# Kernel optimization log

Hardware: AMD Instinct MI355X
Metric: run time of the kernel (lower is better)

Reference implementation:

```python
import jax, jax.numpy as jnp
import numpy as np

NUM_FEATURES = 128
NUM_RADIAL = 6
NUM_ATOM_TYPES = 95
N_ATOMS = 100000
N_EDGES = 1000000


def setup_inputs() -> dict:
    key = jax.random.key(0)
    ks = jax.random.split(key, 8)
    Z = jax.random.randint(ks[0], (N_ATOMS,), 0, NUM_ATOM_TYPES, dtype=jnp.int32)
    rbf = jax.random.normal(ks[1], (N_EDGES, NUM_RADIAL), dtype=jnp.float32)
    idnb_i = jax.random.randint(ks[2], (N_EDGES,), 0, N_ATOMS, dtype=jnp.int32)
    idnb_j = jax.random.randint(ks[3], (N_EDGES,), 0, N_ATOMS, dtype=jnp.int32)
    # parameters
    s3 = np.sqrt(3.0).astype(np.float32)
    embeddings = jax.random.uniform(ks[4], (NUM_ATOM_TYPES, NUM_FEATURES), jnp.float32, -s3, s3)
    W_rbf = jax.random.normal(ks[5], (NUM_RADIAL, NUM_FEATURES), dtype=jnp.float32) * 0.3
    b_rbf = jnp.zeros((NUM_FEATURES,), jnp.float32)
    W = jax.random.normal(ks[6], (2 * NUM_FEATURES + NUM_RADIAL * 0 + 2 * NUM_FEATURES // (2 * NUM_FEATURES) * 0 + 2 * NUM_FEATURES + NUM_FEATURES - 2 * NUM_FEATURES, NUM_FEATURES), dtype=jnp.float32)  # placeholder, replaced below
    W = jax.random.normal(ks[6], (2 * NUM_FEATURES + NUM_FEATURES, NUM_FEATURES), dtype=jnp.float32) * 0.05  # (3F, F)
    b = jnp.zeros((NUM_FEATURES,), jnp.float32)
    return {"Z": Z, "rbf": rbf, "idnb_i": idnb_i, "idnb_j": idnb_j,
            "embeddings": embeddings, "W_rbf": W_rbf, "b_rbf": b_rbf, "W": W, "b": b}


def reference(Z, rbf, idnb_i, idnb_j, embeddings, W_rbf, b_rbf, W, b):
    act = jax.nn.swish
    # dense_rbf: [E, num_radial] -> [E, F]
    rbf_h = act(rbf @ W_rbf + b_rbf)
    # gather atom embeddings by atomic number, then by edge endpoints
    x = embeddings[Z]            # [N_atoms, F]
    x1 = x[idnb_i]               # [E, F]
    x2 = x[idnb_j]               # [E, F]
    h = jnp.concatenate([x1, x2, rbf_h], axis=-1)  # [E, 3F]
    return act(h @ W + b)        # [E, F]
```

## Files before the change

kernel.cpp:

```cpp
#include <hip/hip_runtime.h>
#include <hip/hip_bf16.h>
#include <stdint.h>

#define F 128
#define R 6
#define NTYPES 95
#define MTILE 128
#define HPAD 136

typedef short bf16x8 __attribute__((ext_vector_type(8)));
typedef float floatx4 __attribute__((ext_vector_type(4)));

__device__ __forceinline__ unsigned short f2bf(float x) {
    union { float f; unsigned u; } cv; cv.f = x;
    unsigned u = cv.u;
    return (unsigned short)((u + 0x7FFFu + ((u >> 16) & 1u)) >> 16);
}

__device__ __forceinline__ float swishf(float x) {
    return x / (1.0f + __expf(-x));
}

__global__ void prep_kernel(const float* __restrict__ emb,
                            const float* __restrict__ W,
                            float* __restrict__ embW,
                            unsigned short* __restrict__ w2t) {
    int t = threadIdx.x;
    int b = blockIdx.x;
    if (b < NTYPES) {
        int c = t >> 7, f = t & 127;
        const float* er = emb + b * F;
        const float* Wc = W + c * F * F;
        float a = 0.f;
        #pragma unroll 8
        for (int k = 0; k < F; ++k) a = __builtin_fmaf(er[k], Wc[k * F + f], a);
        embW[b * 256 + c * F + f] = a;
    } else {
        int idx = (b - NTYPES) * 256 + t;
        int n = idx >> 7, k = idx & 127;
        w2t[n * F + k] = f2bf(W[(256 + k) * F + n]);
    }
}

__global__ __launch_bounds__(256) void
edge_kernel(const int* __restrict__ Z,
            const float* __restrict__ rbf,
            const int* __restrict__ idnb_i,
            const int* __restrict__ idnb_j,
            const float* __restrict__ W_rbf,
            const float* __restrict__ b_rbf,
            const float* __restrict__ bvec,
            const float* __restrict__ embW,
            const unsigned short* __restrict__ w2t,
            float* __restrict__ out,
            int E) {
    __shared__ __align__(16) short h_bf[MTILE * HPAD];
    __shared__ float rbf_s[MTILE * R];
    __shared__ int zi_s[MTILE];
    __shared__ int zj_s[MTILE];
    __shared__ float bs[F];

    int t = threadIdx.x;
    int blk = blockIdx.x;
    long ebase = (long)blk * MTILE;

    #pragma unroll
    for (int i = 0; i < 3; ++i) {
        int idx = i * 256 + t;
        long g = ebase * R + idx;
        rbf_s[idx] = (g < (long)E * R) ? rbf[g] : 0.f;
    }
    if (t < MTILE) {
        long e = ebase + t;
        long ec = (e < (long)E) ? e : 0;
        zi_s[t] = Z[idnb_i[ec]];
        zj_s[t] = Z[idnb_j[ec]];
    }
    if (t < F) bs[t] = bvec[t];

    int fpair = t & 63;
    int f0 = fpair * 2;
    float wr0[R], wr1[R];
    #pragma unroll
    for (int r = 0; r < R; ++r) {
        wr0[r] = W_rbf[r * F + f0];
        wr1[r] = W_rbf[r * F + f0 + 1];
    }
    float brb0 = b_rbf[f0], brb1 = b_rbf[f0 + 1];

    __syncthreads();

    int eg = t >> 6;
    for (int it = 0; it < 32; ++it) {
        int e = eg * 32 + it;
        const float* rp = rbf_s + e * R;
        float v0 = brb0, v1 = brb1;
        #pragma unroll
        for (int r = 0; r < R; ++r) {
            float rv = rp[r];
            v0 = __builtin_fmaf(rv, wr0[r], v0);
            v1 = __builtin_fmaf(rv, wr1[r], v1);
        }
        v0 = swishf(v0); v1 = swishf(v1);
        unsigned packed = (unsigned)f2bf(v0) | ((unsigned)f2bf(v1) << 16);
        *(unsigned*)(&h_bf[e * HPAD + f0]) = packed;
    }

    __syncthreads();

    int w = t >> 6;
    int lid = t & 63;
    int quad = lid >> 4;
    int l15 = lid & 15;
    int wbase = w * 32;

    floatx4 acc[2][8];
    #pragma unroll
    for (int rt = 0; rt < 2; ++rt)
        #pragma unroll
        for (int c = 0; c < 8; ++c)
            acc[rt][c] = (floatx4){0.f, 0.f, 0.f, 0.f};

    const bf16x8* w2v = (const bf16x8*)w2t;
    #pragma unroll
    for (int ks = 0; ks < 4; ++ks) {
        bf16x8 a0 = *(const bf16x8*)(&h_bf[(wbase + l15) * HPAD + ks * 32 + quad * 8]);
        bf16x8 a1 = *(const bf16x8*)(&h_bf[(wbase + 16 + l15) * HPAD + ks * 32 + quad * 8]);
        #pragma unroll
        for (int c = 0; c < 8; ++c) {
            bf16x8 bfr = w2v[(c * 16 + l15) * 16 + ks * 4 + quad];
            acc[0][c] = __builtin_amdgcn_mfma_f32_16x16x32_bf16(a0, bfr, acc[0][c], 0, 0, 0);
            acc[1][c] = __builtin_amdgcn_mfma_f32_16x16x32_bf16(a1, bfr, acc[1][c], 0, 0, 0);
        }
    }

    #pragma unroll
    for (int rt = 0; rt < 2; ++rt) {
        #pragma unroll
        for (int rg = 0; rg < 4; ++rg) {
            int e_loc = wbase + rt * 16 + quad * 4 + rg;
            long e_g = ebase + e_loc;
            bool ok = e_g < (long)E;
            int zi = zi_s[e_loc], zj = zj_s[e_loc];
            const float* p0 = embW + zi * 256;
            const float* p1 = embW + zj * 256 + F;
            float* op = out + e_g * F;
            #pragma unroll
            for (int c = 0; c < 8; ++c) {
                int f = c * 16 + l15;
                float v = acc[rt][c][rg] + p0[f] + p1[f] + bs[f];
                v = swishf(v);
                if (ok) op[f] = v;
            }
        }
    }
}

extern "C" void kernel_launch(void* const* d_in, const int* in_sizes, int n_in,
                              void* d_out, int out_size, void* d_ws, size_t ws_size,
                              hipStream_t stream) {
    const int*   Z     = (const int*)d_in[0];
    const float* rbf   = (const float*)d_in[1];
    const int*   id_i  = (const int*)d_in[2];
    const int*   id_j  = (const int*)d_in[3];
    const float* emb   = (const float*)d_in[4];
    const float* W_rbf = (const float*)d_in[5];
    const float* b_rbf = (const float*)d_in[6];
    const float* W     = (const float*)d_in[7];
    const float* bvec  = (const float*)d_in[8];
    float* out = (float*)d_out;
    int E = in_sizes[2];

    float* embW = (float*)d_ws;
    unsigned short* w2t = (unsigned short*)((char*)d_ws + 97280);

    prep_kernel<<<NTYPES + 64, 256, 0, stream>>>(emb, W, embW, w2t);
    int grid = (E + MTILE - 1) / MTILE;
    edge_kernel<<<grid, 256, 0, stream>>>(Z, rbf, id_i, id_j, W_rbf, b_rbf, bvec,
                                          embW, w2t, out, E);
}
```

Baseline: 710.3 us.

## Stage MFMA outputs through LDS for coalesced float4 epilogue stores and fold bias

```diff
diff --git a/kernel.cpp b/kernel.cpp
--- a/kernel.cpp
+++ b/kernel.cpp
@@ -7,6 +7,7 @@
 #define NTYPES 95
 #define MTILE 128
 #define HPAD 136
+#define SPAD 132
 
 typedef short bf16x8 __attribute__((ext_vector_type(8)));
 typedef float floatx4 __attribute__((ext_vector_type(4)));
@@ -18,11 +19,12 @@
 }
 
 __device__ __forceinline__ float swishf(float x) {
-    return x / (1.0f + __expf(-x));
+    return x * __builtin_amdgcn_rcpf(1.0f + __expf(-x));
 }
 
 __global__ void prep_kernel(const float* __restrict__ emb,
                             const float* __restrict__ W,
+                            const float* __restrict__ bvec,
                             float* __restrict__ embW,
                             unsigned short* __restrict__ w2t) {
     int t = threadIdx.x;
@@ -34,6 +36,7 @@
         float a = 0.f;
         #pragma unroll 8
         for (int k = 0; k < F; ++k) a = __builtin_fmaf(er[k], Wc[k * F + f], a);
+        if (c == 0) a += bvec[f];
         embW[b * 256 + c * F + f] = a;
     } else {
         int idx = (b - NTYPES) * 256 + t;
@@ -49,20 +52,20 @@
             const int* __restrict__ idnb_j,
             const float* __restrict__ W_rbf,
             const float* __restrict__ b_rbf,
-            const float* __restrict__ bvec,
             const float* __restrict__ embW,
             const unsigned short* __restrict__ w2t,
             float* __restrict__ out,
             int E) {
-    __shared__ __align__(16) short h_bf[MTILE * HPAD];
+    __shared__ __align__(16) union {
+        short h[MTILE * HPAD];
+        float s[64 * SPAD];
+    } shm;
     __shared__ float rbf_s[MTILE * R];
     __shared__ int zi_s[MTILE];
     __shared__ int zj_s[MTILE];
-    __shared__ float bs[F];
-
-    int t = threadIdx.x;
-    int blk = blockIdx.x;
-    long ebase = (long)blk * MTILE;
+
+    const int t = threadIdx.x;
+    const long ebase = (long)blockIdx.x * MTILE;
 
     #pragma unroll
     for (int i = 0; i < 3; ++i) {
@@ -76,43 +79,56 @@
         zi_s[t] = Z[idnb_i[ec]];
         zj_s[t] = Z[idnb_j[ec]];
     }
-    if (t < F) bs[t] = bvec[t];
-
-    int fpair = t & 63;
-    int f0 = fpair * 2;
-    float wr0[R], wr1[R];
+
+    const int fg = t & 15;
+    const int eg = t >> 4;
+    const int f0 = fg * 8;
+    float wr[R][8], brb[8];
     #pragma unroll
     for (int r = 0; r < R; ++r) {
-        wr0[r] = W_rbf[r * F + f0];
-        wr1[r] = W_rbf[r * F + f0 + 1];
-    }
-    float brb0 = b_rbf[f0], brb1 = b_rbf[f0 + 1];
+        floatx4 a = *(const floatx4*)(W_rbf + r * F + f0);
+        floatx4 b = *(const floatx4*)(W_rbf + r * F + f0 + 4);
+        wr[r][0] = a[0]; wr[r][1] = a[1]; wr[r][2] = a[2]; wr[r][3] = a[3];
+        wr[r][4] = b[0]; wr[r][5] = b[1]; wr[r][6] = b[2]; wr[r][7] = b[3];
+    }
+    {
+        floatx4 a = *(const floatx4*)(b_rbf + f0);
+        floatx4 b = *(const floatx4*)(b_rbf + f0 + 4);
+        brb[0] = a[0]; brb[1] = a[1]; brb[2] = a[2]; brb[3] = a[3];
+        brb[4] = b[0]; brb[5] = b[1]; brb[6] = b[2]; brb[7] = b[3];
+    }
 
     __syncthreads();
 
-    int eg = t >> 6;
-    for (int it = 0; it < 32; ++it) {
-        int e = eg * 32 + it;
-        const float* rp = rbf_s + e * R;
-        float v0 = brb0, v1 = brb1;
-        #pragma unroll
-        for (int r = 0; r < R; ++r) {
-            float rv = rp[r];
-            v0 = __builtin_fmaf(rv, wr0[r], v0);
-            v1 = __builtin_fmaf(rv, wr1[r], v1);
-        }
-        v0 = swishf(v0); v1 = swishf(v1);
-        unsigned packed = (unsigned)f2bf(v0) | ((unsigned)f2bf(v1) << 16);
-        *(unsigned*)(&h_bf[e * HPAD + f0]) = packed;
+    #pragma unroll
+    for (int it = 0; it < 8; ++it) {
+        int e = eg * 8 + it;
+        const float2* rp = (const float2*)(rbf_s + e * R);
+        float2 r01 = rp[0], r23 = rp[1], r45 = rp[2];
+        float rv[R] = {r01.x, r01.y, r23.x, r23.y, r45.x, r45.y};
+        float v[8];
+        #pragma unroll
+        for (int f = 0; f < 8; ++f) v[f] = brb[f];
+        #pragma unroll
+        for (int r = 0; r < R; ++r)
+            #pragma unroll
+            for (int f = 0; f < 8; ++f)
+                v[f] = __builtin_fmaf(rv[r], wr[r][f], v[f]);
+        unsigned pk0 = (unsigned)f2bf(swishf(v[0])) | ((unsigned)f2bf(swishf(v[1])) << 16);
+        unsigned pk1 = (unsigned)f2bf(swishf(v[2])) | ((unsigned)f2bf(swishf(v[3])) << 16);
+        unsigned pk2 = (unsigned)f2bf(swishf(v[4])) | ((unsigned)f2bf(swishf(v[5])) << 16);
+        unsigned pk3 = (unsigned)f2bf(swishf(v[6])) | ((unsigned)f2bf(swishf(v[7])) << 16);
+        uint4 pk; pk.x = pk0; pk.y = pk1; pk.z = pk2; pk.w = pk3;
+        *(uint4*)(&shm.h[e * HPAD + f0]) = pk;
     }
 
     __syncthreads();
 
-    int w = t >> 6;
-    int lid = t & 63;
-    int quad = lid >> 4;
-    int l15 = lid & 15;
-    int wbase = w * 32;
+    const int w = t >> 6;
+    const int lid = t & 63;
+    const int quad = lid >> 4;
+    const int l15 = lid & 15;
+    const int wbase = w * 32;
 
     floatx4 acc[2][8];
     #pragma unroll
@@ -124,8 +140,8 @@
     const bf16x8* w2v = (const bf16x8*)w2t;
     #pragma unroll
     for (int ks = 0; ks < 4; ++ks) {
-        bf16x8 a0 = *(const bf16x8*)(&h_bf[(wbase + l15) * HPAD + ks * 32 + quad * 8]);
-        bf16x8 a1 = *(const bf16x8*)(&h_bf[(wbase + 16 + l15) * HPAD + ks * 32 + quad * 8]);
+        bf16x8 a0 = *(const bf16x8*)(&shm.h[(wbase + l15) * HPAD + ks * 32 + quad * 8]);
+        bf16x8 a1 = *(const bf16x8*)(&shm.h[(wbase + 16 + l15) * HPAD + ks * 32 + quad * 8]);
         #pragma unroll
         for (int c = 0; c < 8; ++c) {
             bf16x8 bfr = w2v[(c * 16 + l15) * 16 + ks * 4 + quad];
@@ -134,25 +150,36 @@
         }
     }
 
+    __syncthreads();
+
     #pragma unroll
     for (int rt = 0; rt < 2; ++rt) {
-        #pragma unroll
-        for (int rg = 0; rg < 4; ++rg) {
-            int e_loc = wbase + rt * 16 + quad * 4 + rg;
+        const int row_w = w * 16 + quad * 4;
+        #pragma unroll
+        for (int c = 0; c < 8; ++c)
+            #pragma unroll
+            for (int rg = 0; rg < 4; ++rg)
+                shm.s[(row_w + rg) * SPAD + c * 16 + l15] = acc[rt][c][rg];
+        __syncthreads();
+
+        #pragma unroll
+        for (int i = 0; i < 8; ++i) {
+            int cid = i * 256 + t;
+            int row_s = cid >> 5;
+            int c4 = (cid & 31) * 4;
+            int e_loc = (row_s >> 4) * 32 + rt * 16 + (row_s & 15);
             long e_g = ebase + e_loc;
-            bool ok = e_g < (long)E;
-            int zi = zi_s[e_loc], zj = zj_s[e_loc];
-            const float* p0 = embW + zi * 256;
-            const float* p1 = embW + zj * 256 + F;
-            float* op = out + e_g * F;
-            #pragma unroll
-            for (int c = 0; c < 8; ++c) {
-                int f = c * 16 + l15;
-                float v = acc[rt][c][rg] + p0[f] + p1[f] + bs[f];
-                v = swishf(v);
-                if (ok) op[f] = v;
+            if (e_g < (long)E) {
+                floatx4 v = *(const floatx4*)(&shm.s[row_s * SPAD + c4]);
+                floatx4 a = *(const floatx4*)(embW + zi_s[e_loc] * 256 + c4);
+                floatx4 b = *(const floatx4*)(embW + zj_s[e_loc] * 256 + F + c4);
+                floatx4 o;
+                #pragma unroll
+                for (int q = 0; q < 4; ++q) o[q] = swishf(v[q] + a[q] + b[q]);
+                *(floatx4*)(out + e_g * F + c4) = o;
             }
         }
+        if (rt == 0) __syncthreads();
     }
 }
 
@@ -174,8 +201,8 @@
     float* embW = (float*)d_ws;
     unsigned short* w2t = (unsigned short*)((char*)d_ws + 97280);
 
-    prep_kernel<<<NTYPES + 64, 256, 0, stream>>>(emb, W, embW, w2t);
+    prep_kernel<<<NTYPES + 64, 256, 0, stream>>>(emb, W, bvec, embW, w2t);
     int grid = (E + MTILE - 1) / MTILE;
-    edge_kernel<<<grid, 256, 0, stream>>>(Z, rbf, id_i, id_j, W_rbf, b_rbf, bvec,
+    edge_kernel<<<grid, 256, 0, stream>>>(Z, rbf, id_i, id_j, W_rbf, b_rbf,
                                           embW, w2t, out, E);
 }
```

After: 731.7 us. 1.03x slower.
